# Optimization experiments

Hardware: AMD Instinct MI355X
Metric: run time of the kernel (lower is better)

## Reference

```python
import jax, jax.numpy as jnp
import numpy as np

B, T, D, H = 4, 2048, 1024, 16
HD = D // H  # 64

def setup_inputs() -> dict:
    key = jax.random.key(0)
    ks = jax.random.split(key, 6)
    s = 0.02
    x = jax.random.normal(ks[0], (B, T, D), dtype=jnp.float32)
    # per-head projection weights, torch Linear layout [out=HD, in=D], stacked over heads
    Wq = jax.random.normal(ks[1], (H, HD, D), dtype=jnp.float32) * s
    Wk = jax.random.normal(ks[2], (H, HD, D), dtype=jnp.float32) * s
    Wv = jax.random.normal(ks[3], (H, HD, D), dtype=jnp.float32) * s
    Wo = jax.random.normal(ks[4], (D, D), dtype=jnp.float32) * s
    bo = jax.random.normal(ks[5], (D,), dtype=jnp.float32) * s
    return {"x": x, "Wq": Wq, "Wk": Wk, "Wv": Wv, "Wo": Wo, "bo": bo}

def reference(x, Wq, Wk, Wv, Wo, bo):
    # per-head projections (same math as per-head nn.Linear, vectorized over heads)
    Q = jnp.einsum('btd,hkd->bhtk', x, Wq)
    K = jnp.einsum('bsd,hkd->bhsk', x, Wk)
    V = jnp.einsum('bsd,hkd->bhsk', x, Wv)
    scale = 1.0 / jnp.sqrt(jnp.asarray(HD, x.dtype))
    logits = jnp.einsum('bhtk,bhsk->bhts', Q, K) * scale  # [B,H,T,S]
    w = jax.nn.softmax(logits, axis=-1)
    out = jnp.einsum('bhts,bhsk->bhtk', w, V)  # [B,H,T,HD]
    # concat heads in order -> [B,T,D]
    cat = jnp.transpose(out, (0, 2, 1, 3)).reshape(B, T, D)
    return cat @ Wo.T + bo
```

## Files before the change

### kernel.cpp

```cpp
#include <hip/hip_runtime.h>
#include <hip/hip_bf16.h>
#include <stdint.h>
#include <math.h>

typedef unsigned short u16;
typedef uint32_t u32;
typedef __bf16 bf16x8 __attribute__((ext_vector_type(8)));
typedef float f32x4 __attribute__((ext_vector_type(4)));
typedef float f32x16 __attribute__((ext_vector_type(16)));
typedef u16 u16x8 __attribute__((ext_vector_type(8)));
typedef u16 u16x4 __attribute__((ext_vector_type(4)));

#define B_ 4
#define T_ 2048
#define D_ 1024
#define H_ 16
#define HD_ 64
#define M_ (B_*T_)

__device__ __forceinline__ u16 f2bf(float f) {
    union { __bf16 h; u16 u; } c;
    c.h = (__bf16)f;
    return c.u;
}

__device__ __forceinline__ void gl16(const u16* g, u16* l) {
    __builtin_amdgcn_global_load_lds(
        (__attribute__((address_space(1))) void*)g,
        (__attribute__((address_space(3))) void*)l, 16, 0, 0);
}

__device__ __forceinline__ f32x4 mfma16(bf16x8 a, bf16x8 b, f32x4 c) {
    return __builtin_amdgcn_mfma_f32_16x16x32_bf16(a, b, c, 0, 0, 0);
}

__device__ __forceinline__ f32x16 mfma32(bf16x8 a, bf16x8 b, f32x16 c) {
    return __builtin_amdgcn_mfma_f32_32x32x16_bf16(a, b, c, 0, 0, 0);
}

__device__ __forceinline__ u32 cvtpk_bf16(float lo, float hi) {
    u32 r;
    asm("v_cvt_pk_bf16_f32 %0, %1, %2" : "=v"(r) : "v"(lo), "v"(hi));
    return r;
}

__device__ __forceinline__ float fexp2(float x) {
    return __builtin_amdgcn_exp2f(x);
}

__device__ __forceinline__ void softmax_pack(
    const f32x16& sacc, float& lp, bf16x8& paA, bf16x8& paB)
{
    float p[16];
#pragma unroll
    for (int r = 0; r < 16; ++r) p[r] = fexp2(sacc[r]);
    float s01 = (p[0] + p[1]) + (p[2] + p[3]);
    float s23 = (p[4] + p[5]) + (p[6] + p[7]);
    float s45 = (p[8] + p[9]) + (p[10] + p[11]);
    float s67 = (p[12] + p[13]) + (p[14] + p[15]);
    lp += (s01 + s23) + (s45 + s67);
    u32 a0 = cvtpk_bf16(p[0], p[1]);
    u32 a1 = cvtpk_bf16(p[2], p[3]);
    u32 b0 = cvtpk_bf16(p[4], p[5]);
    u32 b1 = cvtpk_bf16(p[6], p[7]);
    asm("v_permlane32_swap_b32 %0, %1" : "+v"(a0), "+v"(b0));
    asm("v_permlane32_swap_b32 %0, %1" : "+v"(a1), "+v"(b1));
    union { u32 wq[4]; bf16x8 v; } uA;
    uA.wq[0] = a0; uA.wq[1] = a1; uA.wq[2] = b0; uA.wq[3] = b1;
    paA = uA.v;
    u32 c0 = cvtpk_bf16(p[8], p[9]);
    u32 c1 = cvtpk_bf16(p[10], p[11]);
    u32 d0 = cvtpk_bf16(p[12], p[13]);
    u32 d1 = cvtpk_bf16(p[14], p[15]);
    asm("v_permlane32_swap_b32 %0, %1" : "+v"(c0), "+v"(d0));
    asm("v_permlane32_swap_b32 %0, %1" : "+v"(c1), "+v"(d1));
    union { u32 wq[4]; bf16x8 v; } uB;
    uB.wq[0] = c0; uB.wq[1] = c1; uB.wq[2] = d0; uB.wq[3] = d1;
    paB = uB.v;
}

__global__ __launch_bounds__(256) void precast(
    const float* __restrict__ x,  const float* __restrict__ wq,
    const float* __restrict__ wk, const float* __restrict__ wv,
    const float* __restrict__ wo,
    u16* __restrict__ xb, u16* __restrict__ wqb, u16* __restrict__ wkb,
    u16* __restrict__ wvb, u16* __restrict__ wob)
{
    const int i = (blockIdx.x * 256 + threadIdx.x) * 4;
    const int nx = M_ * D_;
    const float* src; u16* dst; int off;
    if (i < nx) { src = x; dst = xb; off = i; }
    else {
        int j = i - nx;
        int w = j >> 20;
        off = j & ((1 << 20) - 1);
        switch (w) {
            case 0: src = wq; dst = wqb; break;
            case 1: src = wk; dst = wkb; break;
            case 2: src = wv; dst = wvb; break;
            default: src = wo; dst = wob; break;
        }
    }
    float4 v = *(const float4*)&src[off];
    u16x4 p = { f2bf(v.x), f2bf(v.y), f2bf(v.z), f2bf(v.w) };
    *(u16x4*)&dst[off] = p;
}

__device__ __forceinline__ void gemm8_pipe(
    const u16* __restrict__ Xg, const u16* __restrict__ Wg,
    u16* As, u16* Bs,
    const int tid, const int wm, const int wn, const int l15, const int quad,
    f32x4 acc[4][4])
{
    const u16* asrc[4]; int adst[4];
#pragma unroll
    for (int i = 0; i < 4; ++i) {
        int c = tid + i * 512;
        int row = c >> 3, slot = c & 7;
        asrc[i] = Xg + (size_t)row * 1024 + (slot ^ (row & 7)) * 8;
        adst[i] = c * 8;
    }
    const u16* bsrc[2]; int bdst[2];
#pragma unroll
    for (int i = 0; i < 2; ++i) {
        int c = tid + i * 512;
        int row = c >> 3, slot = c & 7;
        bsrc[i] = Wg + (size_t)row * 1024 + (slot ^ (row & 7)) * 8;
        bdst[i] = c * 8;
    }
    const int sw = l15 & 7;
    const int so0 = (quad ^ sw) * 8;
    const int so1 = ((4 + quad) ^ sw) * 8;

#pragma unroll
    for (int tt = 0; tt < 2; ++tt) {
#pragma unroll
        for (int i = 0; i < 4; ++i) gl16(asrc[i] + tt * 64, As + tt * 16384 + adst[i]);
#pragma unroll
        for (int i = 0; i < 2; ++i) gl16(bsrc[i] + tt * 64, Bs + tt * 8192 + bdst[i]);
    }
    asm volatile("s_waitcnt vmcnt(6)" ::: "memory");
    __builtin_amdgcn_s_barrier();

#pragma unroll
    for (int t = 0; t < 16; ++t) {
        const u16* Ab = As + (t % 3) * 16384;
        const u16* Bb = Bs + (t % 3) * 8192;
        if (t + 2 < 16) {
            const int k2 = (t + 2) * 64;
            u16* An = As + ((t + 2) % 3) * 16384;
            u16* Bn = Bs + ((t + 2) % 3) * 8192;
#pragma unroll
            for (int i = 0; i < 4; ++i) gl16(asrc[i] + k2, An + adst[i]);
#pragma unroll
            for (int i = 0; i < 2; ++i) gl16(bsrc[i] + k2, Bn + bdst[i]);
        }
        __builtin_amdgcn_sched_barrier(0);
        bf16x8 af0[4], af1[4], bf0[4], bf1[4];
#pragma unroll
        for (int mf = 0; mf < 4; ++mf) {
            const int rr = (wm * 64 + mf * 16 + l15) * 64;
            af0[mf] = *(const bf16x8*)&Ab[rr + so0];
            af1[mf] = *(const bf16x8*)&Ab[rr + so1];
        }
#pragma unroll
        for (int nf = 0; nf < 4; ++nf) {
            const int rr = (wn * 64 + nf * 16 + l15) * 64;
            bf0[nf] = *(const bf16x8*)&Bb[rr + so0];
            bf1[nf] = *(const bf16x8*)&Bb[rr + so1];
        }
        __builtin_amdgcn_s_setprio(1);
#pragma unroll
        for (int mf = 0; mf < 4; ++mf)
#pragma unroll
            for (int nf = 0; nf < 4; ++nf)
                acc[mf][nf] = mfma16(af0[mf], bf0[nf], acc[mf][nf]);
#pragma unroll
        for (int mf = 0; mf < 4; ++mf)
#pragma unroll
            for (int nf = 0; nf < 4; ++nf)
                acc[mf][nf] = mfma16(af1[mf], bf1[nf], acc[mf][nf]);
        __builtin_amdgcn_s_setprio(0);
        __builtin_amdgcn_sched_barrier(0);
        if (t + 2 < 16)      asm volatile("s_waitcnt vmcnt(6)" ::: "memory");
        else if (t + 1 < 16) asm volatile("s_waitcnt vmcnt(0)" ::: "memory");
        __builtin_amdgcn_s_barrier();
    }
}

__global__ __launch_bounds__(512, 2) void qkv_gemm(
    const u16* __restrict__ Xb, const u16* __restrict__ W3,
    u16* __restrict__ Qo, u16* __restrict__ Ko, u16* __restrict__ Vt)
{
    __shared__ __attribute__((aligned(16))) u16 As[3 * 256 * 64];
    __shared__ __attribute__((aligned(16))) u16 Bs[3 * 128 * 64];

    const int wg = blockIdx.x + 24 * blockIdx.y;
    const int xcd = wg & 7, k = wg >> 3;
    const int by = xcd * 4 + (k / 24);
    const int bx = k % 24;
    const int n0 = bx * 128, m0 = by * 256;
    const u16* Xg = Xb + (size_t)m0 * 1024;
    const u16* Wg = W3 + (size_t)n0 * 1024;
    const int z = n0 >> 10;
    const float qs = (z == 0) ? 0.125f * 1.44269504088896340736f : 1.0f;

    const int tid = threadIdx.x;
    const int lane = tid & 63;
    const int wave = tid >> 6;
    const int wm = wave >> 1, wn = wave & 1;
    const int l15 = lane & 15, quad = lane >> 4;

    f32x4 acc[4][4];
#pragma unroll
    for (int i = 0; i < 4; ++i)
#pragma unroll
        for (int j = 0; j < 4; ++j) acc[i][j] = (f32x4){0.f, 0.f, 0.f, 0.f};

    gemm8_pipe(Xg, Wg, &As[0], &Bs[0], tid, wm, wn, l15, quad, acc);

    if (z == 2) {
#pragma unroll
        for (int mf = 0; mf < 4; ++mf)
#pragma unroll
            for (int nf = 0; nf < 4; ++nf) {
                int row0 = m0 + wm * 64 + mf * 16 + quad * 4;
                int colz = (n0 & 1023) + wn * 64 + nf * 16 + l15;
                int b = row0 >> 11;
                int t = row0 & 2047;
                int h = colz >> 6;
                int hd = colz & 63;
                u16x4 pv = { f2bf(acc[mf][nf][0]), f2bf(acc[mf][nf][1]),
                             f2bf(acc[mf][nf][2]), f2bf(acc[mf][nf][3]) };
                *(u16x4*)&Vt[(((size_t)(b * H_ + h) * HD_ + hd)) * T_ + t] = pv;
            }
    } else {
        u16* Out = (z == 0) ? Qo : Ko;
#pragma unroll
        for (int mf = 0; mf < 4; ++mf)
#pragma unroll
            for (int nf = 0; nf < 4; ++nf)
#pragma unroll
                for (int r = 0; r < 4; ++r) {
                    int row = m0 + wm * 64 + mf * 16 + quad * 4 + r;
                    int colz = (n0 & 1023) + wn * 64 + nf * 16 + l15;
                    int b = row >> 11;
                    int t = row & 2047;
                    int h = colz >> 6;
                    int hd = colz & 63;
                    Out[((b * H_ + h) * T_ + t) * HD_ + hd] = f2bf(acc[mf][nf][r] * qs);
                }
    }
}

__global__ __launch_bounds__(512, 2) void out_gemm(
    const u16* __restrict__ Xb, const u16* __restrict__ W3,
    const float* __restrict__ bias, float* __restrict__ Out)
{
    __shared__ __attribute__((aligned(16))) u16 As[3 * 256 * 64];
    __shared__ __attribute__((aligned(16))) u16 Bs[3 * 128 * 64];

    const int wg = blockIdx.x + 8 * blockIdx.y;
    const int xcd = wg & 7, k = wg >> 3;
    const int by = xcd * 4 + (k / 8);
    const int bx = k & 7;
    const int n0 = bx * 128, m0 = by * 256;
    const u16* Xg = Xb + (size_t)m0 * 1024;
    const u16* Wg = W3 + (size_t)n0 * 1024;

    const int tid = threadIdx.x;
    const int lane = tid & 63;
    const int wave = tid >> 6;
    const int wm = wave >> 1, wn = wave & 1;
    const int l15 = lane & 15, quad = lane >> 4;

    f32x4 acc[4][4];
#pragma unroll
    for (int i = 0; i < 4; ++i)
#pragma unroll
        for (int j = 0; j < 4; ++j) acc[i][j] = (f32x4){0.f, 0.f, 0.f, 0.f};

    gemm8_pipe(Xg, Wg, &As[0], &Bs[0], tid, wm, wn, l15, quad, acc);

#pragma unroll
    for (int mf = 0; mf < 4; ++mf)
#pragma unroll
        for (int nf = 0; nf < 4; ++nf)
#pragma unroll
            for (int r = 0; r < 4; ++r) {
                int row = m0 + wm * 64 + mf * 16 + quad * 4 + r;
                int col = n0 + wn * 64 + nf * 16 + l15;
                Out[(size_t)row * 1024 + col] = acc[mf][nf][r] + bias[col];
            }
}

__global__ __launch_bounds__(256, 2) void attn(
    const u16* __restrict__ Q, const u16* __restrict__ K,
    const u16* __restrict__ Vt_g, u16* __restrict__ O)
{
    __shared__ __attribute__((aligned(16))) u16 Ks[2 * 4096];
    __shared__ __attribute__((aligned(16))) u16 Vts[2 * 4096];
    __shared__ float lps[4 * 64];

    const int tid = threadIdx.x;
    const int lane = tid & 63, w = tid >> 6;
    const int l31 = lane & 31, hi = lane >> 5;

    const int wg = blockIdx.x + (T_ / 256) * (blockIdx.y + H_ * blockIdx.z);
    const int xcd = wg & 7, k8 = wg >> 3;
    const int bh = xcd + 8 * (k8 >> 3);
    const int xq = k8 & 7;
    const int b = bh >> 4, h = bh & 15;
    const int t0 = xq * 256 + w * 64;

    const size_t base = (size_t)bh * T_ * HD_;
    const u16* Kb = K + base;
    const u16* Vtb = Vt_g + base;
    const u16* Qb = Q + base + (size_t)t0 * HD_;

    const int ca = tid,        ra = ca >> 3,  sa = (ca & 7) ^ (ra & 7);
    const int cb2 = tid + 256, rb = cb2 >> 3, sb = (cb2 & 7) ^ (rb & 7);
    const u16* kpa = Kb  + (size_t)ra * 64 + sa * 8;
    const u16* kpb = Kb  + (size_t)rb * 64 + sb * 8;
    const u16* vpa = Vtb + (size_t)ra * T_ + sa * 8;
    const u16* vpb = Vtb + (size_t)rb * T_ + sb * 8;

    int foff[2][4];
#pragma unroll
    for (int nt = 0; nt < 2; ++nt) {
        const int row = nt * 32 + l31;
#pragma unroll
        for (int kb = 0; kb < 4; ++kb)
            foff[nt][kb] = row * 64 + (((kb * 2 + hi) ^ (row & 7)) * 8);
    }

    bf16x8 qf[2][4];
#pragma unroll
    for (int qt = 0; qt < 2; ++qt)
#pragma unroll
        for (int kb = 0; kb < 4; ++kb)
            qf[qt][kb] = *(const bf16x8*)&Qb[(qt * 32 + l31) * 64 + kb * 16 + hi * 8];

    f32x16 zacc;
#pragma unroll
    for (int i = 0; i < 16; ++i) zacc[i] = 0.f;
    f32x16 oacc[2][2];
#pragma unroll
    for (int qt = 0; qt < 2; ++qt)
#pragma unroll
        for (int cb = 0; cb < 2; ++cb) oacc[qt][cb] = zacc;
    float lp[2] = {0.f, 0.f};

    gl16(kpa, &Ks[ca * 8]);
    gl16(kpb, &Ks[cb2 * 8]);
    gl16(vpa, &Vts[ca * 8]);
    gl16(vpb, &Vts[cb2 * 8]);
    asm volatile("s_waitcnt vmcnt(0)" ::: "memory");
    __syncthreads();

    int buf = 0;
    for (int s0 = 0; s0 < T_; s0 += 64) {
        if (s0 + 64 < T_) {
            const int nb = buf ^ 1;
            const size_t ko = (size_t)(s0 + 64) * 64;
            const size_t vo = (size_t)(s0 + 64);
            gl16(kpa + ko, &Ks[nb * 4096 + ca * 8]);
            gl16(kpb + ko, &Ks[nb * 4096 + cb2 * 8]);
            gl16(vpa + vo, &Vts[nb * 4096 + ca * 8]);
            gl16(vpb + vo, &Vts[nb * 4096 + cb2 * 8]);
        }
        const u16* Kc = &Ks[buf * 4096];
        const u16* Vc = &Vts[buf * 4096];

        bf16x8 kf0[4], kf1[4];
#pragma unroll
        for (int kb = 0; kb < 4; ++kb) {
            kf0[kb] = *(const bf16x8*)&Kc[foff[0][kb]];
            kf1[kb] = *(const bf16x8*)&Kc[foff[1][kb]];
        }
        __builtin_amdgcn_s_setprio(1);
        f32x16 s00 = mfma32(kf0[0], qf[0][0], zacc);
        f32x16 s01 = mfma32(kf0[0], qf[1][0], zacc);
        f32x16 s10 = mfma32(kf1[0], qf[0][0], zacc);
        f32x16 s11 = mfma32(kf1[0], qf[1][0], zacc);
#pragma unroll
        for (int kb = 1; kb < 4; ++kb) {
            s00 = mfma32(kf0[kb], qf[0][kb], s00);
            s01 = mfma32(kf0[kb], qf[1][kb], s01);
            s10 = mfma32(kf1[kb], qf[0][kb], s10);
            s11 = mfma32(kf1[kb], qf[1][kb], s11);
        }
        __builtin_amdgcn_s_setprio(0);

        bf16x8 vf[2][4];
#pragma unroll
        for (int cb = 0; cb < 2; ++cb)
#pragma unroll
            for (int kb = 0; kb < 4; ++kb)
                vf[cb][kb] = *(const bf16x8*)&Vc[foff[cb][kb]];

        bf16x8 pa0[2][2], pa1[2][2];
        softmax_pack(s00, lp[0], pa0[0][0], pa0[0][1]);
        softmax_pack(s01, lp[1], pa0[1][0], pa0[1][1]);

        __builtin_amdgcn_s_setprio(1);
#pragma unroll
        for (int cb = 0; cb < 2; ++cb)
#pragma unroll
            for (int kb = 0; kb < 2; ++kb) {
                oacc[0][cb] = mfma32(pa0[0][kb], vf[cb][kb], oacc[0][cb]);
                oacc[1][cb] = mfma32(pa0[1][kb], vf[cb][kb], oacc[1][cb]);
            }
        __builtin_amdgcn_s_setprio(0);

        softmax_pack(s10, lp[0], pa1[0][0], pa1[0][1]);
        softmax_pack(s11, lp[1], pa1[1][0], pa1[1][1]);

        __builtin_amdgcn_s_setprio(1);
#pragma unroll
        for (int cb = 0; cb < 2; ++cb)
#pragma unroll
            for (int kb = 0; kb < 2; ++kb) {
                oacc[0][cb] = mfma32(pa1[0][kb], vf[cb][kb + 2], oacc[0][cb]);
                oacc[1][cb] = mfma32(pa1[1][kb], vf[cb][kb + 2], oacc[1][cb]);
            }
        __builtin_amdgcn_s_setprio(0);

        asm volatile("s_waitcnt vmcnt(0)" ::: "memory");
        __syncthreads();
        buf ^= 1;
    }

#pragma unroll
    for (int qt = 0; qt < 2; ++qt) {
        lp[qt] += __shfl_xor(lp[qt], 32);
        lps[w * 64 + qt * 32 + l31] = lp[qt];
    }
    asm volatile("s_waitcnt lgkmcnt(0)" ::: "memory");

#pragma unroll
    for (int qt = 0; qt < 2; ++qt)
#pragma unroll
        for (int r = 0; r < 16; ++r) {
            const int trow = (r & 3) + 8 * (r >> 2) + 4 * hi;
            const float dn = 1.f / lps[w * 64 + qt * 32 + trow];
            const int t = t0 + qt * 32 + trow;
#pragma unroll
            for (int cb = 0; cb < 2; ++cb) {
                const int col = h * 64 + cb * 32 + l31;
                O[((size_t)b * T_ + t) * D_ + col] = f2bf(oacc[qt][cb][r] * dn);
            }
        }
}

extern "C" void kernel_launch(void* const* d_in, const int* in_sizes, int n_in,
                              void* d_out, int out_size, void* d_ws, size_t ws_size,
                              hipStream_t stream) {
    const float* x  = (const float*)d_in[0];
    const float* Wq = (const float*)d_in[1];
    const float* Wk = (const float*)d_in[2];
    const float* Wv = (const float*)d_in[3];
    const float* Wo = (const float*)d_in[4];
    const float* bo = (const float*)d_in[5];
    float* out = (float*)d_out;

    const size_t n_qkv = (size_t)B_ * H_ * T_ * HD_;
    const size_t n_w   = (size_t)D_ * D_;
    u16* Qw   = (u16*)d_ws;
    u16* Kw   = Qw + n_qkv;
    u16* Vtw  = Kw + n_qkv;
    u16* XbOw = Vtw + n_qkv;
    u16* Xb   = XbOw;
    u16* Ow   = XbOw;
    u16* Wqb  = XbOw + n_qkv;
    u16* Wkb  = Wqb + n_w;
    u16* Wvb  = Wkb + n_w;
    u16* Wob  = Wvb + n_w;

    dim3 gc(12288);
    precast<<<gc, 256, 0, stream>>>(x, Wq, Wk, Wv, Wo, Xb, Wqb, Wkb, Wvb, Wob);

    dim3 g1(3072 / 128, M_ / 256);
    qkv_gemm<<<g1, 512, 0, stream>>>(Xb, Wqb, Qw, Kw, Vtw);

    dim3 g2(T_ / 256, H_, B_);
    attn<<<g2, 256, 0, stream>>>(Qw, Kw, Vtw, Ow);

    dim3 g3(1024 / 128, M_ / 256);
    out_gemm<<<g3, 512, 0, stream>>>(Ow, Wob, bo, out);
}
```

Baseline: 263.7 us.

## Triple-buffer attention K/V tiles with 512-thread blocks and interleaved softmax

The attention kernel moves to 512-thread workgroups that each cover 512 query rows, so a K/V tile loaded into LDS is shared by twice as many waves. The LDS ring goes from two buffers to three, with loads issued two iterations ahead and a partial vmcnt wait, which removes the full drain before each barrier. The QK^T, exp and pack steps are interleaved per key subtile, and V fragments are loaded just before each PV mfma to reduce register pressure. The costs are more LDS per block and fewer blocks in the grid, which could lower occupancy or leave compute units idle in the tail.

```diff
diff --git a/kernel.cpp b/kernel.cpp
--- a/kernel.cpp
+++ b/kernel.cpp
@@ -46,37 +46,6 @@
 
 __device__ __forceinline__ float fexp2(float x) {
     return __builtin_amdgcn_exp2f(x);
-}
-
-__device__ __forceinline__ void softmax_pack(
-    const f32x16& sacc, float& lp, bf16x8& paA, bf16x8& paB)
-{
-    float p[16];
-#pragma unroll
-    for (int r = 0; r < 16; ++r) p[r] = fexp2(sacc[r]);
-    float s01 = (p[0] + p[1]) + (p[2] + p[3]);
-    float s23 = (p[4] + p[5]) + (p[6] + p[7]);
-    float s45 = (p[8] + p[9]) + (p[10] + p[11]);
-    float s67 = (p[12] + p[13]) + (p[14] + p[15]);
-    lp += (s01 + s23) + (s45 + s67);
-    u32 a0 = cvtpk_bf16(p[0], p[1]);
-    u32 a1 = cvtpk_bf16(p[2], p[3]);
-    u32 b0 = cvtpk_bf16(p[4], p[5]);
-    u32 b1 = cvtpk_bf16(p[6], p[7]);
-    asm("v_permlane32_swap_b32 %0, %1" : "+v"(a0), "+v"(b0));
-    asm("v_permlane32_swap_b32 %0, %1" : "+v"(a1), "+v"(b1));
-    union { u32 wq[4]; bf16x8 v; } uA;
-    uA.wq[0] = a0; uA.wq[1] = a1; uA.wq[2] = b0; uA.wq[3] = b1;
-    paA = uA.v;
-    u32 c0 = cvtpk_bf16(p[8], p[9]);
-    u32 c1 = cvtpk_bf16(p[10], p[11]);
-    u32 d0 = cvtpk_bf16(p[12], p[13]);
-    u32 d1 = cvtpk_bf16(p[14], p[15]);
-    asm("v_permlane32_swap_b32 %0, %1" : "+v"(c0), "+v"(d0));
-    asm("v_permlane32_swap_b32 %0, %1" : "+v"(c1), "+v"(d1));
-    union { u32 wq[4]; bf16x8 v; } uB;
-    uB.wq[0] = c0; uB.wq[1] = c1; uB.wq[2] = d0; uB.wq[3] = d1;
-    paB = uB.v;
 }
 
 __global__ __launch_bounds__(256) void precast(
@@ -294,36 +263,34 @@
             }
 }
 
-__global__ __launch_bounds__(256, 2) void attn(
+__global__ __launch_bounds__(512, 2) void attn(
     const u16* __restrict__ Q, const u16* __restrict__ K,
     const u16* __restrict__ Vt_g, u16* __restrict__ O)
 {
-    __shared__ __attribute__((aligned(16))) u16 Ks[2 * 4096];
-    __shared__ __attribute__((aligned(16))) u16 Vts[2 * 4096];
-    __shared__ float lps[4 * 64];
+    __shared__ __attribute__((aligned(16))) u16 Ks[3 * 4096];
+    __shared__ __attribute__((aligned(16))) u16 Vts[3 * 4096];
+    __shared__ float lps[8 * 64];
 
     const int tid = threadIdx.x;
     const int lane = tid & 63, w = tid >> 6;
     const int l31 = lane & 31, hi = lane >> 5;
 
-    const int wg = blockIdx.x + (T_ / 256) * (blockIdx.y + H_ * blockIdx.z);
+    const int wg = blockIdx.x + (T_ / 512) * (blockIdx.y + H_ * blockIdx.z);
     const int xcd = wg & 7, k8 = wg >> 3;
-    const int bh = xcd + 8 * (k8 >> 3);
-    const int xq = k8 & 7;
+    const int bh = xcd + 8 * (k8 >> 2);
+    const int xq = k8 & 3;
     const int b = bh >> 4, h = bh & 15;
-    const int t0 = xq * 256 + w * 64;
+    const int t0 = xq * 512 + w * 64;
 
     const size_t base = (size_t)bh * T_ * HD_;
     const u16* Kb = K + base;
     const u16* Vtb = Vt_g + base;
     const u16* Qb = Q + base + (size_t)t0 * HD_;
 
-    const int ca = tid,        ra = ca >> 3,  sa = (ca & 7) ^ (ra & 7);
-    const int cb2 = tid + 256, rb = cb2 >> 3, sb = (cb2 & 7) ^ (rb & 7);
-    const u16* kpa = Kb  + (size_t)ra * 64 + sa * 8;
-    const u16* kpb = Kb  + (size_t)rb * 64 + sb * 8;
-    const u16* vpa = Vtb + (size_t)ra * T_ + sa * 8;
-    const u16* vpb = Vtb + (size_t)rb * T_ + sb * 8;
+    const int ra = tid >> 3, sa = (tid & 7) ^ (ra & 7);
+    const u16* kp = Kb  + (size_t)ra * 64 + sa * 8;
+    const u16* vp = Vtb + (size_t)ra * T_ + sa * 8;
+    const int ldst = tid * 8;
 
     int foff[2][4];
 #pragma unroll
@@ -351,84 +318,79 @@
         for (int cb = 0; cb < 2; ++cb) oacc[qt][cb] = zacc;
     float lp[2] = {0.f, 0.f};
 
-    gl16(kpa, &Ks[ca * 8]);
-    gl16(kpb, &Ks[cb2 * 8]);
-    gl16(vpa, &Vts[ca * 8]);
-    gl16(vpb, &Vts[cb2 * 8]);
-    asm volatile("s_waitcnt vmcnt(0)" ::: "memory");
-    __syncthreads();
-
-    int buf = 0;
-    for (int s0 = 0; s0 < T_; s0 += 64) {
-        if (s0 + 64 < T_) {
-            const int nb = buf ^ 1;
-            const size_t ko = (size_t)(s0 + 64) * 64;
-            const size_t vo = (size_t)(s0 + 64);
-            gl16(kpa + ko, &Ks[nb * 4096 + ca * 8]);
-            gl16(kpb + ko, &Ks[nb * 4096 + cb2 * 8]);
-            gl16(vpa + vo, &Vts[nb * 4096 + ca * 8]);
-            gl16(vpb + vo, &Vts[nb * 4096 + cb2 * 8]);
-        }
-        const u16* Kc = &Ks[buf * 4096];
-        const u16* Vc = &Vts[buf * 4096];
-
-        bf16x8 kf0[4], kf1[4];
-#pragma unroll
-        for (int kb = 0; kb < 4; ++kb) {
-            kf0[kb] = *(const bf16x8*)&Kc[foff[0][kb]];
-            kf1[kb] = *(const bf16x8*)&Kc[foff[1][kb]];
+#pragma unroll
+    for (int tt = 0; tt < 2; ++tt) {
+        gl16(kp + (size_t)tt * 64 * 64, &Ks[tt * 4096 + ldst]);
+        gl16(vp + (size_t)tt * 64,      &Vts[tt * 4096 + ldst]);
+    }
+    asm volatile("s_waitcnt vmcnt(2)" ::: "memory");
+    __builtin_amdgcn_s_barrier();
+
+    int cur = 0, nx2 = 2;
+    for (int t = 0; t < 32; ++t) {
+        if (t + 2 < 32) {
+            const size_t so = (size_t)(t + 2) * 64;
+            gl16(kp + so * 64, &Ks[nx2 * 4096 + ldst]);
+            gl16(vp + so,      &Vts[nx2 * 4096 + ldst]);
+        }
+        __builtin_amdgcn_sched_barrier(0);
+        const u16* Kc = &Ks[cur * 4096];
+        const u16* Vc = &Vts[cur * 4096];
+
+        bf16x8 pa[2][4];
+#pragma unroll
+        for (int nt = 0; nt < 2; ++nt) {
+            bf16x8 kf[4];
+#pragma unroll
+            for (int kb = 0; kb < 4; ++kb)
+                kf[kb] = *(const bf16x8*)&Kc[foff[nt][kb]];
+#pragma unroll
+            for (int qt = 0; qt < 2; ++qt) {
+                __builtin_amdgcn_s_setprio(1);
+                f32x16 sacc = mfma32(kf[0], qf[qt][0], zacc);
+                sacc = mfma32(kf[1], qf[qt][1], sacc);
+                sacc = mfma32(kf[2], qf[qt][2], sacc);
+                sacc = mfma32(kf[3], qf[qt][3], sacc);
+                __builtin_amdgcn_s_setprio(0);
+                float p[16];
+#pragma unroll
+                for (int r = 0; r < 16; ++r) p[r] = fexp2(sacc[r]);
+                float s01 = (p[0] + p[1]) + (p[2] + p[3]);
+                float s23 = (p[4] + p[5]) + (p[6] + p[7]);
+                float s45 = (p[8] + p[9]) + (p[10] + p[11]);
+                float s67 = (p[12] + p[13]) + (p[14] + p[15]);
+                lp[qt] += (s01 + s23) + (s45 + s67);
+#pragma unroll
+                for (int c = 0; c < 2; ++c) {
+                    const int g = c * 8;
+                    u32 a0 = cvtpk_bf16(p[g + 0], p[g + 1]);
+                    u32 a1 = cvtpk_bf16(p[g + 2], p[g + 3]);
+                    u32 b0 = cvtpk_bf16(p[g + 4], p[g + 5]);
+                    u32 b1 = cvtpk_bf16(p[g + 6], p[g + 7]);
+                    asm("v_permlane32_swap_b32 %0, %1" : "+v"(a0), "+v"(b0));
+                    asm("v_permlane32_swap_b32 %0, %1" : "+v"(a1), "+v"(b1));
+                    union { u32 wq[4]; bf16x8 v; } uu;
+                    uu.wq[0] = a0; uu.wq[1] = a1; uu.wq[2] = b0; uu.wq[3] = b1;
+                    pa[qt][nt * 2 + c] = uu.v;
+                }
+            }
         }
         __builtin_amdgcn_s_setprio(1);
-        f32x16 s00 = mfma32(kf0[0], qf[0][0], zacc);
-        f32x16 s01 = mfma32(kf0[0], qf[1][0], zacc);
-        f32x16 s10 = mfma32(kf1[0], qf[0][0], zacc);
-        f32x16 s11 = mfma32(kf1[0], qf[1][0], zacc);
-#pragma unroll
-        for (int kb = 1; kb < 4; ++kb) {
-            s00 = mfma32(kf0[kb], qf[0][kb], s00);
-            s01 = mfma32(kf0[kb], qf[1][kb], s01);
-            s10 = mfma32(kf1[kb], qf[0][kb], s10);
-            s11 = mfma32(kf1[kb], qf[1][kb], s11);
-        }
-        __builtin_amdgcn_s_setprio(0);
-
-        bf16x8 vf[2][4];
 #pragma unroll
         for (int cb = 0; cb < 2; ++cb)
 #pragma unroll
-            for (int kb = 0; kb < 4; ++kb)
-                vf[cb][kb] = *(const bf16x8*)&Vc[foff[cb][kb]];
-
-        bf16x8 pa0[2][2], pa1[2][2];
-        softmax_pack(s00, lp[0], pa0[0][0], pa0[0][1]);
-        softmax_pack(s01, lp[1], pa0[1][0], pa0[1][1]);
-
-        __builtin_amdgcn_s_setprio(1);
-#pragma unroll
-        for (int cb = 0; cb < 2; ++cb)
-#pragma unroll
-            for (int kb = 0; kb < 2; ++kb) {
-                oacc[0][cb] = mfma32(pa0[0][kb], vf[cb][kb], oacc[0][cb]);
-                oacc[1][cb] = mfma32(pa0[1][kb], vf[cb][kb], oacc[1][cb]);
+            for (int kb = 0; kb < 4; ++kb) {
+                bf16x8 vf = *(const bf16x8*)&Vc[foff[cb][kb]];
+                oacc[0][cb] = mfma32(pa[0][kb], vf, oacc[0][cb]);
+                oacc[1][cb] = mfma32(pa[1][kb], vf, oacc[1][cb]);
             }
         __builtin_amdgcn_s_setprio(0);
-
-        softmax_pack(s10, lp[0], pa1[0][0], pa1[0][1]);
-        softmax_pack(s11, lp[1], pa1[1][0], pa1[1][1]);
-
-        __builtin_amdgcn_s_setprio(1);
-#pragma unroll
-        for (int cb = 0; cb < 2; ++cb)
-#pragma unroll
-            for (int kb = 0; kb < 2; ++kb) {
-                oacc[0][cb] = mfma32(pa1[0][kb], vf[cb][kb + 2], oacc[0][cb]);
-                oacc[1][cb] = mfma32(pa1[1][kb], vf[cb][kb + 2], oacc[1][cb]);
-            }
-        __builtin_amdgcn_s_setprio(0);
-
-        asm volatile("s_waitcnt vmcnt(0)" ::: "memory");
-        __syncthreads();
-        buf ^= 1;
+        __builtin_amdgcn_sched_barrier(0);
+        if (t + 2 < 32)      asm volatile("s_waitcnt vmcnt(2)" ::: "memory");
+        else if (t + 1 < 32) asm volatile("s_waitcnt vmcnt(0)" ::: "memory");
+        __builtin_amdgcn_s_barrier();
+        cur = (cur == 2) ? 0 : cur + 1;
+        nx2 = (nx2 == 2) ? 0 : nx2 + 1;
     }
 
 #pragma unroll
@@ -483,8 +445,8 @@
     dim3 g1(3072 / 128, M_ / 256);
     qkv_gemm<<<g1, 512, 0, stream>>>(Xb, Wqb, Qw, Kw, Vtw);
 
-    dim3 g2(T_ / 256, H_, B_);
-    attn<<<g2, 256, 0, stream>>>(Qw, Kw, Vtw, Ow);
+    dim3 g2(T_ / 512, H_, B_);
+    attn<<<g2, 512, 0, stream>>>(Qw, Kw, Vtw, Ow);
 
     dim3 g3(1024 / 128, M_ / 256);
     out_gemm<<<g3, 512, 0, stream>>>(Ow, Wob, bo, out);
```

New measurement: 268.3 us. No clear change (+1.7%).
